# Performance work log

Measured on AMD Instinct MI355X. Metric: run time of the kernel, lower is better.

## Reference

```python
import jax, jax.numpy as jnp
import numpy as np

N_NODES = 100000
N_EDGES = 1600000
MSG = 128
EPS = 1e-12  # F.normalize default eps


def setup_inputs() -> dict:
    key = jax.random.key(0)
    ks = jax.random.split(key, 12)
    s = 1.0 / np.sqrt(MSG)
    inp = {
        "x": jax.random.normal(ks[0], (N_NODES, 3), dtype=jnp.float32),
        "m_ij": jax.random.normal(ks[1], (N_EDGES, MSG), dtype=jnp.float32),
        "edges": jax.random.randint(ks[2], (2, N_EDGES), 0, N_NODES, dtype=jnp.int64),
        # weigths MLP: Linear(MSG,MSG) -> SiLU -> Linear(MSG,1)
        "Ww1": jax.random.uniform(ks[3], (MSG, MSG), jnp.float32, -s, s),
        "bw1": jax.random.uniform(ks[4], (MSG,), jnp.float32, -s, s),
        "Ww2": jax.random.uniform(ks[5], (MSG, 1), jnp.float32, -s, s),
        "bw2": jax.random.uniform(ks[6], (1,), jnp.float32, -s, s),
        # attention MLP: Linear(MSG,MSG) -> SiLU -> Linear(MSG,1)
        "Wa1": jax.random.uniform(ks[7], (MSG, MSG), jnp.float32, -s, s),
        "ba1": jax.random.uniform(ks[8], (MSG,), jnp.float32, -s, s),
        "Wa2": jax.random.uniform(ks[9], (MSG, 1), jnp.float32, -s, s),
        "ba2": jax.random.uniform(ks[10], (1,), jnp.float32, -s, s),
    }
    return inp


def reference(x, m_ij, edges, Ww1, bw1, Ww2, bw2, Wa1, ba1, Wa2, ba2):
    n_nodes = x.shape[0]
    src = edges[0]  # receiver index (scatter target)
    dst = edges[1]  # neighbor index

    # w_ij = MLP(m_ij) -> [E, 1]
    w_ij = jax.nn.silu(m_ij @ Ww1 + bw1) @ Ww2 + bw2

    # attention: a_ij = exp(MLP(m_ij)); normalized per receiver node (softmax-like)
    a_ij = jnp.exp(jax.nn.silu(m_ij @ Wa1 + ba1) @ Wa2 + ba2)  # [E, 1]
    a_i = jax.ops.segment_sum(a_ij, src, num_segments=n_nodes)  # [N, 1]
    w_ij = w_ij * (a_ij / a_i[src])

    # normalized position differences, weighted
    d = x[dst] - x[src]  # [E, 3]
    norm = jnp.maximum(jnp.linalg.norm(d, axis=1, keepdims=True), EPS)
    x_ij = (d / norm) * w_ij

    x_diff = jax.ops.segment_sum(x_ij, src, num_segments=n_nodes)  # [N, 3]
    return x + x_diff
```

## Files before the change

### kernel.cpp

```cpp
#include <hip/hip_runtime.h>
#include <cmath>

#define MSG 128
#define TILE 64
#define TPB 256
#define NB_MAX 512

typedef __attribute__((ext_vector_type(8))) __bf16 bf16x8;
typedef __attribute__((ext_vector_type(4))) float f32x4;

__device__ __forceinline__ unsigned short f2bf(float f) {
  union { float f; unsigned u; } v; v.f = f;
  unsigned r = v.u + 0x7FFFu + ((v.u >> 16) & 1u);
  return (unsigned short)(r >> 16);
}

__global__ void prep_weights_kernel(const float* __restrict__ Ww1,
                                    const float* __restrict__ Wa1,
                                    unsigned short* __restrict__ WtW,
                                    unsigned short* __restrict__ WtA) {
  int idx = blockIdx.x * blockDim.x + threadIdx.x;
  if (idx < MSG * MSG) {
    int k = idx >> 7;
    int n = idx & 127;
    WtW[n * MSG + k] = f2bf(Ww1[idx]);
    WtA[n * MSG + k] = f2bf(Wa1[idx]);
  }
}

__device__ __forceinline__ void gload_lds16(const float* g, float* l) {
  __builtin_amdgcn_global_load_lds(
      (const __attribute__((address_space(1))) void*)g,
      (__attribute__((address_space(3))) void*)l, 16, 0, 0);
}

__global__ __launch_bounds__(TPB, 2)
void edge_mlp_pipe_kernel(const float* __restrict__ m_ij,
                          const unsigned short* __restrict__ WtW,
                          const unsigned short* __restrict__ WtA,
                          const float* __restrict__ bw1, const float* __restrict__ Ww2,
                          const float* __restrict__ bw2,
                          const float* __restrict__ ba1, const float* __restrict__ Wa2,
                          const float* __restrict__ ba2,
                          const int* __restrict__ src,
                          const int* __restrict__ dst,
                          const float* __restrict__ x,
                          float* __restrict__ num4, int E, int ntiles) {
  __shared__ __align__(16) float buf[2][TILE * MSG];
  __shared__ float plds[2][4][TILE];

  const int tid = threadIdx.x;
  const int w = tid >> 6;
  const int lane = tid & 63;
  const int quad = lane >> 4;
  const int l16 = lane & 15;

  bf16x8 wf[2][2][4];
  f32x4 c1[2][2], c2[2][2];
  #pragma unroll
  for (int nt = 0; nt < 2; ++nt) {
    const int unit16 = w * 32 + nt * 16;
    const size_t ro = (size_t)(unit16 + l16) * MSG + quad * 8;
    #pragma unroll
    for (int kt = 0; kt < 4; ++kt) {
      wf[nt][0][kt] = *(const bf16x8*)(WtW + ro + kt * 32);
      wf[nt][1][kt] = *(const bf16x8*)(WtA + ro + kt * 32);
    }
    const int co = unit16 + quad * 4;
    c1[nt][0] = *(const f32x4*)(bw1 + co);
    c2[nt][0] = *(const f32x4*)(Ww2 + co);
    c1[nt][1] = *(const f32x4*)(ba1 + co);
    c2[nt][1] = *(const f32x4*)(Wa2 + co);
  }
  const float bw2s = bw2[0], ba2s = ba2[0];

  auto stage = [&](int tile, int bsel) {
    #pragma unroll
    for (int i = 0; i < 8; ++i) {
      const int chunk = i * TPB + tid;
      const int db = chunk * 16;
      const int row = db >> 9;
      const int col = db & 511;
      const int scol = col ^ ((row & 7) << 4);
      int grow = tile * TILE + row;
      if (grow >= E) grow = E - 1;
      const float* g = m_ij + (size_t)grow * MSG + (scol >> 2);
      gload_lds16(g, &buf[bsel][0] + (db >> 2));
    }
  };

  int tt = blockIdx.x;
  if (tt < ntiles) stage(tt, 0);
  asm volatile("s_waitcnt vmcnt(0)" ::: "memory");
  __builtin_amdgcn_s_barrier();
  int cur = 0;

  for (; tt < ntiles; tt += gridDim.x) {
    const int nxt = tt + (int)gridDim.x;
    if (nxt < ntiles) stage(nxt, cur ^ 1);

    const int eL = w * 16 + l16;
    const int ge = tt * TILE + eL;
    const bool fown = (quad == 0) && (ge < E);
    int sN = 0, dN = 0;
    float sx = 0.f, sy = 0.f, sz = 0.f, gx = 0.f, gy = 0.f, gz = 0.f;
    if (fown) { sN = src[ge]; dN = dst[ge]; }
    if (fown) {
      sx = x[3 * sN]; sy = x[3 * sN + 1]; sz = x[3 * sN + 2];
      gx = x[3 * dN]; gy = x[3 * dN + 1]; gz = x[3 * dN + 2];
    }

    #pragma unroll
    for (int et = 0; et < 4; ++et) {
      const int row = et * 16 + l16;
      const int rbase = row * MSG;
      const int xorf = (row & 7) << 2;
      bf16x8 bf[4];
      #pragma unroll
      for (int kt = 0; kt < 4; ++kt) {
        const int c0 = quad * 8 + kt * 32;
        const f32x4 v0 = *(const f32x4*)(&buf[cur][rbase + (c0 ^ xorf)]);
        const f32x4 v1 = *(const f32x4*)(&buf[cur][rbase + ((c0 + 4) ^ xorf)]);
        bf16x8 f;
        f[0] = (__bf16)v0.x; f[1] = (__bf16)v0.y;
        f[2] = (__bf16)v0.z; f[3] = (__bf16)v0.w;
        f[4] = (__bf16)v1.x; f[5] = (__bf16)v1.y;
        f[6] = (__bf16)v1.z; f[7] = (__bf16)v1.w;
        bf[kt] = f;
      }
      f32x4 acc[2][2];
      #pragma unroll
      for (int nt = 0; nt < 2; ++nt) {
        acc[nt][0] = {0.f, 0.f, 0.f, 0.f};
        acc[nt][1] = {0.f, 0.f, 0.f, 0.f};
      }
      #pragma unroll
      for (int kt = 0; kt < 4; ++kt) {
        #pragma unroll
        for (int nt = 0; nt < 2; ++nt) {
          acc[nt][0] = __builtin_amdgcn_mfma_f32_16x16x32_bf16(wf[nt][0][kt], bf[kt], acc[nt][0], 0, 0, 0);
          acc[nt][1] = __builtin_amdgcn_mfma_f32_16x16x32_bf16(wf[nt][1][kt], bf[kt], acc[nt][1], 0, 0, 0);
        }
      }
      float pW = 0.f, pA = 0.f;
      #pragma unroll
      for (int nt = 0; nt < 2; ++nt) {
        #pragma unroll
        for (int r = 0; r < 4; ++r) {
          const float hw = acc[nt][0][r] + c1[nt][0][r];
          const float ha = acc[nt][1][r] + c1[nt][1][r];
          pW += (hw * c2[nt][0][r]) * __builtin_amdgcn_rcpf(1.f + __expf(-hw));
          pA += (ha * c2[nt][1][r]) * __builtin_amdgcn_rcpf(1.f + __expf(-ha));
        }
      }
      pW += __shfl_xor(pW, 16, 64); pW += __shfl_xor(pW, 32, 64);
      pA += __shfl_xor(pA, 16, 64); pA += __shfl_xor(pA, 32, 64);
      if (quad == 0) {
        plds[0][w][et * 16 + l16] = pW;
        plds[1][w][et * 16 + l16] = pA;
      }
    }

    asm volatile("s_waitcnt lgkmcnt(0)" ::: "memory");
    __builtin_amdgcn_s_barrier();

    if (fown) {
      const float sW = plds[0][0][eL] + plds[0][1][eL] + plds[0][2][eL] + plds[0][3][eL];
      const float sA = plds[1][0][eL] + plds[1][1][eL] + plds[1][2][eL] + plds[1][3][eL];
      const float a = __expf(sA + ba2s);
      const float t = (sW + bw2s) * a;
      const float dx = gx - sx, dy = gy - sy, dz = gz - sz;
      const float nrm = sqrtf(dx * dx + dy * dy + dz * dz);
      const float inv = t * __builtin_amdgcn_rcpf(fmaxf(nrm, 1e-12f));
      float* basep = num4 + (size_t)4 * sN;
      atomicAdd(basep + 0, dx * inv);
      atomicAdd(basep + 1, dy * inv);
      atomicAdd(basep + 2, dz * inv);
      atomicAdd(basep + 3, a);
    }

    asm volatile("s_waitcnt vmcnt(4) lgkmcnt(0)" ::: "memory");
    __builtin_amdgcn_s_barrier();
    cur ^= 1;
  }
}

__global__ void finalize_kernel(const float* __restrict__ x,
                                const f32x4* __restrict__ num4,
                                float* __restrict__ out, int N) {
  int n = blockIdx.x * blockDim.x + threadIdx.x;
  if (n >= N) return;
  const f32x4 v = num4[n];
  const float inv = (v[3] != 0.f) ? __builtin_amdgcn_rcpf(v[3]) : 0.f;
  out[3 * n + 0] = x[3 * n + 0] + v[0] * inv;
  out[3 * n + 1] = x[3 * n + 1] + v[1] * inv;
  out[3 * n + 2] = x[3 * n + 2] + v[2] * inv;
}

extern "C" void kernel_launch(void* const* d_in, const int* in_sizes, int n_in,
                              void* d_out, int out_size, void* d_ws, size_t ws_size,
                              hipStream_t stream) {
  const float* x    = (const float*)d_in[0];
  const float* m_ij = (const float*)d_in[1];
  const int*   edges = (const int*)d_in[2];
  const float* Ww1 = (const float*)d_in[3];
  const float* bw1 = (const float*)d_in[4];
  const float* Ww2 = (const float*)d_in[5];
  const float* bw2 = (const float*)d_in[6];
  const float* Wa1 = (const float*)d_in[7];
  const float* ba1 = (const float*)d_in[8];
  const float* Wa2 = (const float*)d_in[9];
  const float* ba2 = (const float*)d_in[10];

  const int N = in_sizes[0] / 3;
  const int E = in_sizes[1] / MSG;
  const int* src = edges;
  const int* dst = edges + E;

  char* p = (char*)d_ws;
  unsigned short* WtW = (unsigned short*)p; p += (size_t)MSG * MSG * 2;
  unsigned short* WtA = (unsigned short*)p; p += (size_t)MSG * MSG * 2;
  float* num4 = (float*)p; p += (size_t)N * 4 * 4;

  float* out = (float*)d_out;

  const int ntiles = (E + TILE - 1) / TILE;
  const int nb = ntiles < NB_MAX ? ntiles : NB_MAX;

  hipMemsetAsync(num4, 0, (size_t)N * 4 * 4, stream);
  prep_weights_kernel<<<(MSG * MSG + 255) / 256, 256, 0, stream>>>(Ww1, Wa1, WtW, WtA);
  edge_mlp_pipe_kernel<<<nb, TPB, 0, stream>>>(
      m_ij, WtW, WtA, bw1, Ww2, bw2, ba1, Wa2, ba2, src, dst, x, num4, E, ntiles);
  finalize_kernel<<<(N + 255) / 256, 256, 0, stream>>>(x, (const f32x4*)num4, out, N);
}
```

Baseline: 1.238 ms.

## Halve edge tile, raise occupancy, and prefetch next tile's edge gathers

Tile size drops from 64 to 32 edges. The grid cap and launch-bounds occupancy hint go up, so more blocks stay resident per CU. The src/dst index loads and the x-coordinate gathers for the next tile are now issued a tile ahead, with hand-tuned vmcnt waits, so their latency overlaps the current tile's MFMA work instead of stalling it. The atomic scatter now runs on 8 lanes per wave with a validity mask, and every iteration stages a (possibly redundant) tile. The costs are more per-tile overhead, including barriers and weight-fragment reuse over fewer edges, and the fragile explicit vmcnt counting.

Measured after the change: 1.204 ms. 2.7% less time.

```diff
diff --git a/kernel.cpp b/kernel.cpp
--- a/kernel.cpp
+++ b/kernel.cpp
@@ -2,9 +2,9 @@
 #include <cmath>
 
 #define MSG 128
-#define TILE 64
+#define TILE 32
 #define TPB 256
-#define NB_MAX 512
+#define NB_MAX 768
 
 typedef __attribute__((ext_vector_type(8))) __bf16 bf16x8;
 typedef __attribute__((ext_vector_type(4))) float f32x4;
@@ -34,7 +34,7 @@
       (__attribute__((address_space(3))) void*)l, 16, 0, 0);
 }
 
-__global__ __launch_bounds__(TPB, 2)
+__global__ __launch_bounds__(TPB, 3)
 void edge_mlp_pipe_kernel(const float* __restrict__ m_ij,
                           const unsigned short* __restrict__ WtW,
                           const unsigned short* __restrict__ WtA,
@@ -76,7 +76,7 @@
 
   auto stage = [&](int tile, int bsel) {
     #pragma unroll
-    for (int i = 0; i < 8; ++i) {
+    for (int i = 0; i < 4; ++i) {
       const int chunk = i * TPB + tid;
       const int db = chunk * 16;
       const int row = db >> 9;
@@ -84,38 +84,45 @@
       const int scol = col ^ ((row & 7) << 4);
       int grow = tile * TILE + row;
       if (grow >= E) grow = E - 1;
-      const float* g = m_ij + (size_t)grow * MSG + (scol >> 2);
-      gload_lds16(g, &buf[bsel][0] + (db >> 2));
+      gload_lds16(m_ij + (size_t)grow * MSG + (scol >> 2), &buf[bsel][0] + (db >> 2));
     }
   };
 
+  const int fid = w * 8 + (lane & 7);
+
   int tt = blockIdx.x;
-  if (tt < ntiles) stage(tt, 0);
-  asm volatile("s_waitcnt vmcnt(0)" ::: "memory");
+  int ge = tt * TILE + fid;
+  bool vcur = (ge < E);
+  int gec = vcur ? ge : 0;
+  int sN = src[gec];
+  int dN = dst[gec];
+  asm volatile("" ::: "memory");
+  stage(tt, 0);
+  asm volatile("s_waitcnt vmcnt(4)" ::: "memory");
+  float sx = x[3 * sN], sy = x[3 * sN + 1], sz = x[3 * sN + 2];
+  float gx = x[3 * dN], gy = x[3 * dN + 1], gz = x[3 * dN + 2];
+  asm volatile("s_waitcnt vmcnt(6)" ::: "memory");
   __builtin_amdgcn_s_barrier();
   int cur = 0;
 
   for (; tt < ntiles; tt += gridDim.x) {
     const int nxt = tt + (int)gridDim.x;
-    if (nxt < ntiles) stage(nxt, cur ^ 1);
-
-    const int eL = w * 16 + l16;
-    const int ge = tt * TILE + eL;
-    const bool fown = (quad == 0) && (ge < E);
-    int sN = 0, dN = 0;
-    float sx = 0.f, sy = 0.f, sz = 0.f, gx = 0.f, gy = 0.f, gz = 0.f;
-    if (fown) { sN = src[ge]; dN = dst[ge]; }
-    if (fown) {
-      sx = x[3 * sN]; sy = x[3 * sN + 1]; sz = x[3 * sN + 2];
-      gx = x[3 * dN]; gy = x[3 * dN + 1]; gz = x[3 * dN + 2];
-    }
+    const int snxt = (nxt < ntiles) ? nxt : (ntiles - 1);
+
+    const int geN = snxt * TILE + fid;
+    const bool vnxt = (geN < E);
+    const int geNc = vnxt ? geN : 0;
+    const int sN2 = src[geNc];
+    const int dN2 = dst[geNc];
+    asm volatile("" ::: "memory");
+    stage(snxt, cur ^ 1);
 
     #pragma unroll
-    for (int et = 0; et < 4; ++et) {
+    for (int et = 0; et < 2; ++et) {
       const int row = et * 16 + l16;
       const int rbase = row * MSG;
       const int xorf = (row & 7) << 2;
-      bf16x8 bf[4];
+      bf16x8 bfv[4];
       #pragma unroll
       for (int kt = 0; kt < 4; ++kt) {
         const int c0 = quad * 8 + kt * 32;
@@ -126,7 +133,7 @@
         f[2] = (__bf16)v0.z; f[3] = (__bf16)v0.w;
         f[4] = (__bf16)v1.x; f[5] = (__bf16)v1.y;
         f[6] = (__bf16)v1.z; f[7] = (__bf16)v1.w;
-        bf[kt] = f;
+        bfv[kt] = f;
       }
       f32x4 acc[2][2];
       #pragma unroll
@@ -138,8 +145,8 @@
       for (int kt = 0; kt < 4; ++kt) {
         #pragma unroll
         for (int nt = 0; nt < 2; ++nt) {
-          acc[nt][0] = __builtin_amdgcn_mfma_f32_16x16x32_bf16(wf[nt][0][kt], bf[kt], acc[nt][0], 0, 0, 0);
-          acc[nt][1] = __builtin_amdgcn_mfma_f32_16x16x32_bf16(wf[nt][1][kt], bf[kt], acc[nt][1], 0, 0, 0);
+          acc[nt][0] = __builtin_amdgcn_mfma_f32_16x16x32_bf16(wf[nt][0][kt], bfv[kt], acc[nt][0], 0, 0, 0);
+          acc[nt][1] = __builtin_amdgcn_mfma_f32_16x16x32_bf16(wf[nt][1][kt], bfv[kt], acc[nt][1], 0, 0, 0);
         }
       }
       float pW = 0.f, pA = 0.f;
@@ -164,23 +171,40 @@
     asm volatile("s_waitcnt lgkmcnt(0)" ::: "memory");
     __builtin_amdgcn_s_barrier();
 
-    if (fown) {
-      const float sW = plds[0][0][eL] + plds[0][1][eL] + plds[0][2][eL] + plds[0][3][eL];
-      const float sA = plds[1][0][eL] + plds[1][1][eL] + plds[1][2][eL] + plds[1][3][eL];
+    asm volatile("s_waitcnt vmcnt(6)" ::: "memory");
+
+    {
+      float sW = 0.f, sA = 0.f;
+      #pragma unroll
+      for (int ww = 0; ww < 4; ++ww) {
+        sW += plds[0][ww][fid];
+        sA += plds[1][ww][fid];
+      }
       const float a = __expf(sA + ba2s);
       const float t = (sW + bw2s) * a;
       const float dx = gx - sx, dy = gy - sy, dz = gz - sz;
       const float nrm = sqrtf(dx * dx + dy * dy + dz * dz);
       const float inv = t * __builtin_amdgcn_rcpf(fmaxf(nrm, 1e-12f));
-      float* basep = num4 + (size_t)4 * sN;
-      atomicAdd(basep + 0, dx * inv);
-      atomicAdd(basep + 1, dy * inv);
-      atomicAdd(basep + 2, dz * inv);
-      atomicAdd(basep + 3, a);
-    }
-
-    asm volatile("s_waitcnt vmcnt(4) lgkmcnt(0)" ::: "memory");
+      const float m = vcur ? 1.f : 0.f;
+      if (quad == 0 && l16 < 8) {
+        float* basep = num4 + (size_t)4 * sN;
+        atomicAdd(basep + 0, dx * inv * m);
+        atomicAdd(basep + 1, dy * inv * m);
+        atomicAdd(basep + 2, dz * inv * m);
+        atomicAdd(basep + 3, a * m);
+      }
+    }
+
+    asm volatile("s_waitcnt vmcnt(8)" ::: "memory");
+    const float sx2 = x[3 * sN2], sy2 = x[3 * sN2 + 1], sz2 = x[3 * sN2 + 2];
+    const float gx2 = x[3 * dN2], gy2 = x[3 * dN2 + 1], gz2 = x[3 * dN2 + 2];
+
+    asm volatile("s_waitcnt vmcnt(10) lgkmcnt(0)" ::: "memory");
     __builtin_amdgcn_s_barrier();
+
+    sN = sN2; dN = dN2; vcur = vnxt;
+    sx = sx2; sy = sy2; sz = sz2;
+    gx = gx2; gy = gy2; gz = gz2;
     cur ^= 1;
   }
 }
```
